# Performance work log

Hardware: AMD Instinct MI355X
Metric: run time of the kernel (lower is better)

Reference implementation:

```python
import jax, jax.numpy as jnp
import numpy as np

THRESHOLD = 0.3
EPS = 1e-8  # matches torch F.cosine_similarity eps


def _normalize(x):
    # L2-normalize rows with torch-style eps clamp on the norm
    n = jnp.sqrt(jnp.sum(x * x, axis=-1, keepdims=True))
    return x / jnp.maximum(n, EPS)


def _triu_cos_self(x):
    # pairwise cosine similarity of x with itself, upper triangle (offset=1)
    xn = _normalize(x)
    csm = xn @ xn.T  # [N, N]
    i, j = jnp.triu_indices(x.shape[0], k=1)
    return csm[i, j]


def setup_inputs() -> dict:
    key = jax.random.key(0)
    k1, k2 = jax.random.split(key)
    stereos = jax.random.normal(k1, (96, 768), dtype=jnp.float32)
    astereos = jax.random.normal(k2, (96, 768), dtype=jnp.float32)
    return {"stereos": stereos, "astereos": astereos}


def reference(stereos, astereos):
    # positive sims: triu of each self cosine-similarity matrix, concatenated
    pos_sim = jnp.concatenate(
        [_triu_cos_self(stereos), _triu_cos_self(astereos)], axis=0
    )  # [P]
    # negative sims: full cross cosine similarity, flattened
    neg = _normalize(astereos) @ _normalize(stereos).T  # [M, N]
    neg_sim = neg.reshape(-1)  # [Q]
    # hinge over the full pos x neg outer product: mean(max(0, neg - pos + thr))
    diff = neg_sim[None, :] - pos_sim[:, None] + THRESHOLD  # [P, Q]
    return jnp.mean(jnp.maximum(diff, 0.0))
```

## Files before the change

kernel.cpp:

```cpp
#include <hip/hip_runtime.h>
#include <math.h>

#define NROWS    96
#define DIM      768
#define THRESH   0.3f
#define NPAIR    4560
#define PTOT     9120
#define QTOT     9216
#define SPR      24
#define NBLK_SC  576
#define NBLK_A   300
#define NBLK_TOT 876
#define GRPSZ    24
#define NGRP     37

#define AST(p, v) __hip_atomic_store((p), (v), __ATOMIC_RELAXED, __HIP_MEMORY_SCOPE_AGENT)
#define ALD(p)    __hip_atomic_load((p), __ATOMIC_RELAXED, __HIP_MEMORY_SCOPE_AGENT)


__device__ __forceinline__ float d12(
    const float4& x0, const float4& x1, const float4& x2,
    const float4& y0, const float4& y1, const float4& y2)
{
    return x0.x*y0.x + x0.y*y0.y + x0.z*y0.z + x0.w*y0.w
         + x1.x*y1.x + x1.y*y1.y + x1.z*y1.z + x1.w*y1.w
         + x2.x*y2.x + x2.y*y2.y + x2.z*y2.z + x2.w*y2.w;
}

template <int N>
__device__ __forceinline__ void wreduce(float* v)
{
#pragma unroll
    for (int off = 32; off; off >>= 1) {
#pragma unroll
        for (int k = 0; k < N; k++) v[k] += __shfl_down(v[k], off);
    }
}

__global__ __launch_bounds__(256) void fused_kernel(
    const float* __restrict__ stereos, const float* __restrict__ astereos,
    float* __restrict__ pos, float* __restrict__ neg,
    float* __restrict__ slotSp, float* __restrict__ slotSn,
    float* __restrict__ slotMx, float* __restrict__ slotMn,
    unsigned int* __restrict__ gctr0, unsigned int* __restrict__ sctr,
    const unsigned int* __restrict__ ref, float* __restrict__ out)
{
    __shared__ float  sSp[4], sSn[4], sMx[4], sMn[4];
    __shared__ int    sLast;
    __shared__ double rsp[4], rsn[4], redd[4];
    __shared__ float  rmx[4], rmn[4];
    __shared__ double bcd[2];
    __shared__ float  bnmin;
    __shared__ int    rare;
    __shared__ float  sNeg[QTOT];

    int tid  = threadIdx.x;
    int wave = tid >> 6, lane = tid & 63;

    unsigned int base = 0;
    if (tid == 0) base = ALD(ref);

    float wsp = 0.f, wsn = 0.f, wmx = -INFINITY, wmn = INFINITY;

    if (blockIdx.x < NBLK_SC) {
        int gw = blockIdx.x * 4 + wave;
        int i  = gw / SPR;
        int j0 = (gw - i * SPR) * 4;
        float acc[13];
        {
            const float4* aS = (const float4*)(stereos  + i * DIM);
            const float4* aC = (const float4*)(astereos + i * DIM);
            float4 as0 = aS[lane], as1 = aS[lane + 64], as2 = aS[lane + 128];
            float4 ac0 = aC[lane], ac1 = aC[lane + 64], ac2 = aC[lane + 128];
            acc[0] = d12(as0, as1, as2, as0, as1, as2);
            acc[1] = d12(ac0, ac1, ac2, ac0, ac1, ac2);
#pragma unroll
            for (int m = 0; m < 4; m++) {
                const float4* b = (const float4*)(stereos + (j0 + m) * DIM);
                float4 b0 = b[lane], b1 = b[lane + 64], b2 = b[lane + 128];
                acc[2 + m]  = d12(b0, b1, b2, b0, b1, b2);
                acc[6 + m]  = d12(as0, as1, as2, b0, b1, b2);
                acc[10 + m] = d12(ac0, ac1, ac2, b0, b1, b2);
            }
            wreduce<13>(acc);
        }
        if (lane == 0) {
            float invaS = 1.0f / fmaxf(sqrtf(acc[0]), 1e-8f);
            float invaC = 1.0f / fmaxf(sqrtf(acc[1]), 1e-8f);
            int baseS = (i * (191 - i)) / 2 - i - 1;
#pragma unroll
            for (int m = 0; m < 4; m++) {
                float invb = 1.0f / fmaxf(sqrtf(acc[2 + m]), 1e-8f);
                float sc = acc[10 + m] * invaC * invb;
                AST(&neg[i * NROWS + j0 + m], sc);
                wsn += sc; wmn = fminf(wmn, sc);
                if (j0 + m > i) {
                    float ss = acc[6 + m] * invaS * invb;
                    AST(&pos[baseS + j0 + m], ss);
                    wsp += ss; wmx = fmaxf(wmx, ss);
                }
            }
        }
    } else {
        int aw = (blockIdx.x - NBLK_SC) * 4 + wave;
        int s = 0;
        {
            int r = aw;
            while (r >= 4 * s + 4) { r -= 4 * s + 4; s++; }
            aw = r;
        }
        int ia = aw, ja0 = 4 * s;
        float accA[9];
        {
            const float4* aA = (const float4*)(astereos + ia * DIM);
            float4 a0 = aA[lane], a1 = aA[lane + 64], a2 = aA[lane + 128];
            accA[0] = d12(a0, a1, a2, a0, a1, a2);
#pragma unroll
            for (int m = 0; m < 4; m++) {
                const float4* b = (const float4*)(astereos + (ja0 + m) * DIM);
                float4 b0 = b[lane], b1 = b[lane + 64], b2 = b[lane + 128];
                accA[1 + m] = d12(b0, b1, b2, b0, b1, b2);
                accA[5 + m] = d12(a0, a1, a2, b0, b1, b2);
            }
            wreduce<9>(accA);
        }
        if (lane == 0) {
            float invaA = 1.0f / fmaxf(sqrtf(accA[0]), 1e-8f);
            int baseA = (ia * (191 - ia)) / 2 - ia - 1;
#pragma unroll
            for (int m = 0; m < 4; m++) {
                if (ja0 + m > ia) {
                    float invb = 1.0f / fmaxf(sqrtf(accA[1 + m]), 1e-8f);
                    float sa = accA[5 + m] * invaA * invb;
                    AST(&pos[NPAIR + baseA + ja0 + m], sa);
                    wsp += sa; wmx = fmaxf(wmx, sa);
                }
            }
        }
    }

    if (lane == 0) { sSp[wave] = wsp; sSn[wave] = wsn;
                     sMx[wave] = wmx; sMn[wave] = wmn; }
    __syncthreads();

    if (tid == 0) {
        AST(&slotSp[blockIdx.x], sSp[0] + sSp[1] + sSp[2] + sSp[3]);
        AST(&slotSn[blockIdx.x], sSn[0] + sSn[1] + sSn[2] + sSn[3]);
        AST(&slotMx[blockIdx.x], fmaxf(fmaxf(sMx[0], sMx[1]), fmaxf(sMx[2], sMx[3])));
        AST(&slotMn[blockIdx.x], fminf(fminf(sMn[0], sMn[1]), fminf(sMn[2], sMn[3])));
        asm volatile("s_waitcnt vmcnt(0)" ::: "memory");
        int g = blockIdx.x / GRPSZ;
        unsigned int cnt = (unsigned int)min(GRPSZ, NBLK_TOT - g * GRPSZ);
        unsigned int* gctr = (unsigned int*)((char*)gctr0 + (size_t)g * 2048);
        unsigned int old = atomicAdd(gctr, 1u);
        int win = 0;
        if (((old - base) % cnt) == cnt - 1u) {
            unsigned int old2 = atomicAdd(sctr, 1u);
            win = (((old2 - base) % (unsigned)NGRP) == (unsigned)(NGRP - 1));
        }
        sLast = win;
    }
    __syncthreads();
    if (!sLast) return;

    double sp = 0.0, sn = 0.0;
    float mx = -INFINITY, mn = INFINITY;
    for (int f = tid; f < NBLK_TOT; f += 256) {
        sp += (double)ALD(&slotSp[f]);
        sn += (double)ALD(&slotSn[f]);
        mx = fmaxf(mx, ALD(&slotMx[f]));
        mn = fminf(mn, ALD(&slotMn[f]));
    }
    for (int off = 32; off; off >>= 1) {
        sp += __shfl_down(sp, off);
        sn += __shfl_down(sn, off);
        mx = fmaxf(mx, __shfl_down(mx, off));
        mn = fminf(mn, __shfl_down(mn, off));
    }
    if (lane == 0) { rsp[wave] = sp; rsn[wave] = sn;
                     rmx[wave] = mx; rmn[wave] = mn; }
    __syncthreads();
    if (tid == 0) {
        bcd[0] = rsp[0] + rsp[1] + rsp[2] + rsp[3];
        bcd[1] = rsn[0] + rsn[1] + rsn[2] + rsn[3];
        float pm = fmaxf(fmaxf(rmx[0], rmx[1]), fmaxf(rmx[2], rmx[3]));
        float nm = fminf(fminf(rmn[0], rmn[1]), fminf(rmn[2], rmn[3]));
        bnmin = nm;
        rare = (pm - nm > THRESH) ? 1 : 0;
    }
    __syncthreads();

    double corr = 0.0;
    if (rare) {
        for (int q = tid; q < QTOT; q += 256) sNeg[q] = ALD(&neg[q]);
        __syncthreads();
        float nmv = bnmin;
        for (int p = tid; p < PTOT; p += 256) {
            float pv = ALD(&pos[p]);
            if (pv - nmv > THRESH) {
                for (int q = 0; q < QTOT; q++) {
                    float d = pv - THRESH - sNeg[q];
                    if (d > 0.f) corr += (double)d;
                }
            }
        }
    }
    for (int off = 32; off; off >>= 1) corr += __shfl_down(corr, off);
    if (lane == 0) redd[wave] = corr;
    __syncthreads();
    if (tid == 0) {
        corr = redd[0] + redd[1] + redd[2] + redd[3];
        double PQ = (double)PTOT * (double)QTOT;
        double total = (double)PTOT * bcd[1] - (double)QTOT * bcd[0]
                     + PQ * (double)THRESH + corr;
        out[0] = (float)(total / PQ);
    }
}

extern "C" void kernel_launch(void* const* d_in, const int* in_sizes, int n_in,
                              void* d_out, int out_size, void* d_ws, size_t ws_size,
                              hipStream_t stream)
{
    const float* stereos  = (const float*)d_in[0];
    const float* astereos = (const float*)d_in[1];

    char* ws = (char*)d_ws;
    float* pos    = (float*)ws;
    float* neg    = (float*)(ws + 36480);
    float* slotSp = (float*)(ws + 73344);
    float* slotSn = (float*)(ws + 77440);
    float* slotMx = (float*)(ws + 81536);
    float* slotMn = (float*)(ws + 85632);

    size_t gctr_off, sctr_off, ref_off;
    if (ws_size >= (1u << 19) + 4) {
        gctr_off = (size_t)1 << 18;
        sctr_off = (size_t)7 << 16;
        ref_off  = (size_t)1 << 19;
    } else {
        gctr_off = 89856;
        sctr_off = 89984;
        ref_off  = 90112;
    }
    unsigned int* gctr0 = (unsigned int*)(ws + gctr_off);
    unsigned int* sctr  = (unsigned int*)(ws + sctr_off);
    const unsigned int* ref = (const unsigned int*)(ws + ref_off);

    fused_kernel<<<NBLK_TOT, 256, 0, stream>>>(stereos, astereos, pos, neg,
                                               slotSp, slotSn, slotMx, slotMn,
                                               gctr0, sctr, ref, (float*)d_out);
}
```

Baseline: 60.22 us.

## Drop per-element pos/neg stores, pack block partials, recompute sims in rare path

Stops writing every positive and negative similarity to global memory in the main path and packs the four per-block partials into two 64-bit stores and loads. The rare correction path, taken only when max pos minus min neg exceeds the threshold, now recomputes norms and similarities from the inputs in the last block instead of reading stored values. It also removes the 36 KB shared neg buffer, which may improve occupancy. The cost is a very slow serial fallback when the rare path triggers, and for these random inputs the threshold condition is likely true, so that fallback may run.

Result: no change. 60.98 us (+1.3%).

```diff
diff --git a/kernel.cpp b/kernel.cpp
--- a/kernel.cpp
+++ b/kernel.cpp
@@ -14,8 +14,10 @@
 #define GRPSZ    24
 #define NGRP     37
 
-#define AST(p, v) __hip_atomic_store((p), (v), __ATOMIC_RELAXED, __HIP_MEMORY_SCOPE_AGENT)
-#define ALD(p)    __hip_atomic_load((p), __ATOMIC_RELAXED, __HIP_MEMORY_SCOPE_AGENT)
+#define AST64(p, v) __hip_atomic_store((p), (v), __ATOMIC_RELAXED, __HIP_MEMORY_SCOPE_AGENT)
+#define ALD64(p)    __hip_atomic_load((p), __ATOMIC_RELAXED, __HIP_MEMORY_SCOPE_AGENT)
+#define ASTF(p, v)  __hip_atomic_store((p), (v), __ATOMIC_RELAXED, __HIP_MEMORY_SCOPE_AGENT)
+#define ALDF(p)     __hip_atomic_load((p), __ATOMIC_RELAXED, __HIP_MEMORY_SCOPE_AGENT)
 
 
 __device__ __forceinline__ float d12(
@@ -37,11 +39,15 @@
     }
 }
 
+__device__ __forceinline__ unsigned long long pack2(float a, float b)
+{
+    return (unsigned long long)__float_as_uint(a)
+         | ((unsigned long long)__float_as_uint(b) << 32);
+}
+
 __global__ __launch_bounds__(256) void fused_kernel(
     const float* __restrict__ stereos, const float* __restrict__ astereos,
-    float* __restrict__ pos, float* __restrict__ neg,
-    float* __restrict__ slotSp, float* __restrict__ slotSn,
-    float* __restrict__ slotMx, float* __restrict__ slotMn,
+    unsigned long long* __restrict__ slot2, float* __restrict__ scratch,
     unsigned int* __restrict__ gctr0, unsigned int* __restrict__ sctr,
     const unsigned int* __restrict__ ref, float* __restrict__ out)
 {
@@ -52,13 +58,13 @@
     __shared__ double bcd[2];
     __shared__ float  bnmin;
     __shared__ int    rare;
-    __shared__ float  sNeg[QTOT];
+    __shared__ float  invn[192];
 
     int tid  = threadIdx.x;
     int wave = tid >> 6, lane = tid & 63;
 
     unsigned int base = 0;
-    if (tid == 0) base = ALD(ref);
+    if (tid == 0) base = ALD64(ref);
 
     float wsp = 0.f, wsn = 0.f, wmx = -INFINITY, wmn = INFINITY;
 
@@ -87,16 +93,13 @@
         if (lane == 0) {
             float invaS = 1.0f / fmaxf(sqrtf(acc[0]), 1e-8f);
             float invaC = 1.0f / fmaxf(sqrtf(acc[1]), 1e-8f);
-            int baseS = (i * (191 - i)) / 2 - i - 1;
 #pragma unroll
             for (int m = 0; m < 4; m++) {
                 float invb = 1.0f / fmaxf(sqrtf(acc[2 + m]), 1e-8f);
                 float sc = acc[10 + m] * invaC * invb;
-                AST(&neg[i * NROWS + j0 + m], sc);
                 wsn += sc; wmn = fminf(wmn, sc);
                 if (j0 + m > i) {
                     float ss = acc[6 + m] * invaS * invb;
-                    AST(&pos[baseS + j0 + m], ss);
                     wsp += ss; wmx = fmaxf(wmx, ss);
                 }
             }
@@ -126,13 +129,11 @@
         }
         if (lane == 0) {
             float invaA = 1.0f / fmaxf(sqrtf(accA[0]), 1e-8f);
-            int baseA = (ia * (191 - ia)) / 2 - ia - 1;
 #pragma unroll
             for (int m = 0; m < 4; m++) {
                 if (ja0 + m > ia) {
                     float invb = 1.0f / fmaxf(sqrtf(accA[1 + m]), 1e-8f);
                     float sa = accA[5 + m] * invaA * invb;
-                    AST(&pos[NPAIR + baseA + ja0 + m], sa);
                     wsp += sa; wmx = fmaxf(wmx, sa);
                 }
             }
@@ -144,10 +145,12 @@
     __syncthreads();
 
     if (tid == 0) {
-        AST(&slotSp[blockIdx.x], sSp[0] + sSp[1] + sSp[2] + sSp[3]);
-        AST(&slotSn[blockIdx.x], sSn[0] + sSn[1] + sSn[2] + sSn[3]);
-        AST(&slotMx[blockIdx.x], fmaxf(fmaxf(sMx[0], sMx[1]), fmaxf(sMx[2], sMx[3])));
-        AST(&slotMn[blockIdx.x], fminf(fminf(sMn[0], sMn[1]), fminf(sMn[2], sMn[3])));
+        float spB = sSp[0] + sSp[1] + sSp[2] + sSp[3];
+        float snB = sSn[0] + sSn[1] + sSn[2] + sSn[3];
+        float mxB = fmaxf(fmaxf(sMx[0], sMx[1]), fmaxf(sMx[2], sMx[3]));
+        float mnB = fminf(fminf(sMn[0], sMn[1]), fminf(sMn[2], sMn[3]));
+        AST64(&slot2[blockIdx.x * 2 + 0], pack2(spB, snB));
+        AST64(&slot2[blockIdx.x * 2 + 1], pack2(mxB, mnB));
         asm volatile("s_waitcnt vmcnt(0)" ::: "memory");
         int g = blockIdx.x / GRPSZ;
         unsigned int cnt = (unsigned int)min(GRPSZ, NBLK_TOT - g * GRPSZ);
@@ -166,10 +169,12 @@
     double sp = 0.0, sn = 0.0;
     float mx = -INFINITY, mn = INFINITY;
     for (int f = tid; f < NBLK_TOT; f += 256) {
-        sp += (double)ALD(&slotSp[f]);
-        sn += (double)ALD(&slotSn[f]);
-        mx = fmaxf(mx, ALD(&slotMx[f]));
-        mn = fminf(mn, ALD(&slotMn[f]));
+        unsigned long long v0 = ALD64(&slot2[f * 2 + 0]);
+        unsigned long long v1 = ALD64(&slot2[f * 2 + 1]);
+        sp += (double)__uint_as_float((unsigned)v0);
+        sn += (double)__uint_as_float((unsigned)(v0 >> 32));
+        mx = fmaxf(mx, __uint_as_float((unsigned)v1));
+        mn = fminf(mn, __uint_as_float((unsigned)(v1 >> 32)));
     }
     for (int off = 32; off; off >>= 1) {
         sp += __shfl_down(sp, off);
@@ -192,15 +197,49 @@
 
     double corr = 0.0;
     if (rare) {
-        for (int q = tid; q < QTOT; q += 256) sNeg[q] = ALD(&neg[q]);
+        for (int r = tid; r < 192; r += 256) {
+            const float* row = (r < NROWS) ? stereos + r * DIM
+                                           : astereos + (r - NROWS) * DIM;
+            float s = 0.f;
+            for (int k = 0; k < DIM; k++) s += row[k] * row[k];
+            invn[r] = 1.0f / fmaxf(sqrtf(s), 1e-8f);
+        }
+        __syncthreads();
+        for (int q = tid; q < QTOT; q += 256) {
+            int ai = q / NROWS, sj = q - ai * NROWS;
+            const float* ra = astereos + ai * DIM;
+            const float* rs = stereos  + sj * DIM;
+            float s = 0.f;
+            for (int k = 0; k < DIM; k++) s += ra[k] * rs[k];
+            ASTF(&scratch[q], s * invn[NROWS + ai] * invn[sj]);
+        }
+        asm volatile("s_waitcnt vmcnt(0)" ::: "memory");
         __syncthreads();
         float nmv = bnmin;
-        for (int p = tid; p < PTOT; p += 256) {
-            float pv = ALD(&pos[p]);
-            if (pv - nmv > THRESH) {
-                for (int q = 0; q < QTOT; q++) {
-                    float d = pv - THRESH - sNeg[q];
-                    if (d > 0.f) corr += (double)d;
+        for (int i = 0; i < NROWS - 1; i++) {
+            int cnt2 = NROWS - 1 - i;
+            for (int jj = tid; jj < cnt2; jj += 256) {
+                int j = i + 1 + jj;
+                const float* si = stereos + i * DIM;
+                const float* sj = stereos + j * DIM;
+                const float* ai = astereos + i * DIM;
+                const float* aj = astereos + j * DIM;
+                float ds = 0.f, da = 0.f;
+                for (int k = 0; k < DIM; k++) {
+                    ds += si[k] * sj[k];
+                    da += ai[k] * aj[k];
+                }
+                float pv[2];
+                pv[0] = ds * invn[i] * invn[j];
+                pv[1] = da * invn[NROWS + i] * invn[NROWS + j];
+#pragma unroll
+                for (int t = 0; t < 2; t++) {
+                    if (pv[t] - nmv > THRESH) {
+                        for (int q = 0; q < QTOT; q++) {
+                            float d = pv[t] - THRESH - ALDF(&scratch[q]);
+                            if (d > 0.f) corr += (double)d;
+                        }
+                    }
                 }
             }
         }
@@ -225,15 +264,11 @@
     const float* astereos = (const float*)d_in[1];
 
     char* ws = (char*)d_ws;
-    float* pos    = (float*)ws;
-    float* neg    = (float*)(ws + 36480);
-    float* slotSp = (float*)(ws + 73344);
-    float* slotSn = (float*)(ws + 77440);
-    float* slotMx = (float*)(ws + 81536);
-    float* slotMn = (float*)(ws + 85632);
+    float* scratch = (float*)ws;
+    unsigned long long* slot2 = (unsigned long long*)(ws + 73344);
 
     size_t gctr_off, sctr_off, ref_off;
-    if (ws_size >= (1u << 19) + 4) {
+    if (ws_size >= (1u << 19) + 8) {
         gctr_off = (size_t)1 << 18;
         sctr_off = (size_t)7 << 16;
         ref_off  = (size_t)1 << 19;
@@ -246,7 +281,7 @@
     unsigned int* sctr  = (unsigned int*)(ws + sctr_off);
     const unsigned int* ref = (const unsigned int*)(ws + ref_off);
 
-    fused_kernel<<<NBLK_TOT, 256, 0, stream>>>(stereos, astereos, pos, neg,
-                                               slotSp, slotSn, slotMx, slotMn,
-                                               gctr0, sctr, ref, (float*)d_out);
-}
+    fused_kernel<<<NBLK_TOT, 256, 0, stream>>>(stereos, astereos, slot2,
+                                               scratch, gctr0, sctr, ref,
+                                               (float*)d_out);
+}
```
